# Performance work log

Hardware: AMD Instinct MI355X
Metric: run time of the kernel (lower is better)

## Reference

```python
import jax, jax.numpy as jnp
import numpy as np

N, E, D, R = 50000, 600000, 128, 8


def setup_inputs() -> dict:
    key = jax.random.key(0)
    ks = jax.random.split(key, 10)
    return {
        "x": jax.random.normal(ks[0], (N, D), dtype=jnp.float32),
        "h": jax.random.normal(ks[1], (N, D), dtype=jnp.float32),
        "edge_index": jax.random.randint(ks[2], (2, E), 0, N, dtype=jnp.int32),
        "edge_type": jax.random.randint(ks[3], (E,), 0, R, dtype=jnp.int32),
        "edge_weight": jax.random.uniform(ks[4], (E,), dtype=jnp.float32),
        "rel_weight": jax.random.normal(ks[5], (R, D, D), dtype=jnp.float32) * 0.05,
        "root_weight": jax.random.normal(ks[6], (D, D), dtype=jnp.float32) * 0.05,
        "bias": jax.random.normal(ks[7], (D,), dtype=jnp.float32) * 0.05,
        "skip_weight": jax.random.normal(ks[8], (D, D), dtype=jnp.float32) * 0.05,
        "skip_bias": jax.random.normal(ks[9], (D,), dtype=jnp.float32) * 0.05,
    }


def reference(x, h, edge_index, edge_type, edge_weight, rel_weight, root_weight, bias, skip_weight, skip_bias):
    # skip projection (nn.Linear: y = x W^T + b)
    skip = x @ skip_weight.T + skip_bias  # [N, D]

    src, dst = edge_index[0], edge_index[1]  # PyG: message from src (x_j), aggregated at dst

    # Transform every node by every relation once (R is small), then gather per edge.
    # Avoids per-edge [E, D, D] weight gather.
    h_rel = jnp.einsum('nd,rdf->nrf', h, rel_weight)  # [N, R, D]
    msg = h_rel[src, edge_type] * edge_weight[:, None]  # [E, D]

    agg = jax.ops.segment_sum(msg, dst, num_segments=h.shape[0])  # [N, D]

    out = agg + h @ root_weight + bias + skip
    return out
```

## Files before the change

kernel.cpp:

```cpp
#include <hip/hip_runtime.h>


constexpr int DIM  = 128;
constexpr int BM   = 64;
constexpr int KC   = 32;
constexpr int BPAD = 4;
constexpr int KTOT = 1280;
constexpr int SCAN_CHUNK = 2048;

typedef __attribute__((ext_vector_type(8))) short     short8v;
typedef __attribute__((ext_vector_type(8))) unsigned short ushort8v;
typedef __attribute__((ext_vector_type(4))) float     float4v;

__device__ __forceinline__ unsigned short f2bf(float x) {
    union { float f; unsigned u; } c; c.f = x;
    unsigned u = c.u;
    u += 0x7fffu + ((u >> 16) & 1u);
    return (unsigned short)(u >> 16);
}

__global__ __launch_bounds__(256) void zero_i32_kernel(int* __restrict__ p, int n)
{
    int i = blockIdx.x * 256 + threadIdx.x;
    if (i < n) p[i] = 0;
}

__global__ __launch_bounds__(256) void hist_kernel(
    const int* __restrict__ ei, int* __restrict__ counts, int E)
{
    int e = blockIdx.x * 256 + threadIdx.x;
    if (e < E) atomicAdd(&counts[ei[(long long)E + e]], 1);
}

__global__ __launch_bounds__(256) void scan1_kernel(
    const int* __restrict__ counts, int* __restrict__ local,
    int* __restrict__ blockSums, int N)
{
    __shared__ int sh[256];
    const int b = blockIdx.x, t = threadIdx.x;
    const int base = b * SCAN_CHUNK + t * 8;

    int v[8];
    int s = 0;
    #pragma unroll
    for (int j = 0; j < 8; ++j) {
        int idx = base + j;
        v[j] = (idx < N) ? counts[idx] : 0;
        s += v[j];
    }
    sh[t] = s;
    __syncthreads();
    for (int off = 1; off < 256; off <<= 1) {
        int x = (t >= off) ? sh[t - off] : 0;
        __syncthreads();
        sh[t] += x;
        __syncthreads();
    }
    int ex = sh[t] - s;
    if (t == 255) blockSums[b] = sh[255];
    #pragma unroll
    for (int j = 0; j < 8; ++j) {
        int idx = base + j;
        if (idx < N) { local[idx] = ex; ex += v[j]; }
    }
}

__global__ __launch_bounds__(1024) void scan2_kernel(int* __restrict__ bs, int nb)
{
    __shared__ int sh[1024];
    const int t = threadIdx.x;
    int v = (t < nb) ? bs[t] : 0;
    sh[t] = v;
    __syncthreads();
    for (int off = 1; off < 1024; off <<= 1) {
        int x = (t >= off) ? sh[t - off] : 0;
        __syncthreads();
        sh[t] += x;
        __syncthreads();
    }
    if (t < nb) bs[t] = sh[t] - v;
}

__global__ __launch_bounds__(256) void scan3_kernel(
    int* __restrict__ offsets, const int* __restrict__ blockSums,
    int* __restrict__ cursor, int N, int E)
{
    const int b = blockIdx.x, t = threadIdx.x;
    const int add = blockSums[b];
    #pragma unroll
    for (int j = 0; j < 8; ++j) {
        int idx = b * SCAN_CHUNK + j * 256 + t;
        if (idx < N) {
            int v = offsets[idx] + add;
            offsets[idx] = v;
            cursor[idx]  = v;
        }
    }
    if (b == 0 && t == 0) offsets[N] = E;
}

__global__ __launch_bounds__(256) void scatter_kernel(
    const int* __restrict__ ei, const int* __restrict__ et,
    const float* __restrict__ ew, int* __restrict__ cursor,
    int* __restrict__ spack, float* __restrict__ sw, int E)
{
    int e = blockIdx.x * 256 + threadIdx.x;
    if (e < E) {
        int pos = atomicAdd(&cursor[ei[(long long)E + e]], 1);
        spack[pos] = (ei[e] << 3) | (et[e] & 7);
        sw[pos]    = ew[e];
    }
}

__global__ __launch_bounds__(256) void accum_kernel(
    const int* __restrict__ spack, const float* __restrict__ sw,
    const float* __restrict__ h, const int* __restrict__ offsets,
    unsigned short* __restrict__ S, int N)
{
    const int n    = blockIdx.x * 4 + (threadIdx.x >> 6);
    const int lane = threadIdx.x & 63;
    if (n >= N) return;

    const int start = offsets[n];
    const int end   = offsets[n + 1];

    float2 acc[8];
    #pragma unroll
    for (int rr = 0; rr < 8; ++rr) acc[rr] = make_float2(0.f, 0.f);

    int o = start;
    for (; o + 2 <= end; o += 2) {
        const int   p0 = spack[o],     p1 = spack[o + 1];
        const float w0 = sw[o],        w1 = sw[o + 1];
        const float2 h0 = *reinterpret_cast<const float2*>(
            h + (size_t)(p0 >> 3) * DIM + lane * 2);
        const float2 h1 = *reinterpret_cast<const float2*>(
            h + (size_t)(p1 >> 3) * DIM + lane * 2);
        const int r0 = p0 & 7, r1 = p1 & 7;
        #pragma unroll
        for (int rr = 0; rr < 8; ++rr) {
            const float m0 = (rr == r0) ? w0 : 0.f;
            const float m1 = (rr == r1) ? w1 : 0.f;
            acc[rr].x += m0 * h0.x + m1 * h1.x;
            acc[rr].y += m0 * h0.y + m1 * h1.y;
        }
    }
    if (o < end) {
        const int   p0 = spack[o];
        const float w0 = sw[o];
        const float2 h0 = *reinterpret_cast<const float2*>(
            h + (size_t)(p0 >> 3) * DIM + lane * 2);
        const int r0 = p0 & 7;
        #pragma unroll
        for (int rr = 0; rr < 8; ++rr) {
            const float m0 = (rr == r0) ? w0 : 0.f;
            acc[rr].x += m0 * h0.x;
            acc[rr].y += m0 * h0.y;
        }
    }

    #pragma unroll
    for (int rr = 0; rr < 8; ++rr) {
        unsigned pk = (unsigned)f2bf(acc[rr].x) | ((unsigned)f2bf(acc[rr].y) << 16);
        *reinterpret_cast<unsigned*>(
            &S[(size_t)n * 1024 + rr * DIM + lane * 2]) = pk;
    }
}

__global__ __launch_bounds__(256) void repack_B_kernel(
    const float* __restrict__ relF, const float* __restrict__ rootW,
    const float* __restrict__ skipW, unsigned short* __restrict__ Bt)
{
    int idx = blockIdx.x * 256 + threadIdx.x;
    if (idx >= DIM * KTOT) return;
    int f = idx / KTOT, k = idx % KTOT;
    float v;
    if (k < 1024)       v = relF[(size_t)k * DIM + f];
    else if (k < 1152)  v = rootW[(k - 1024) * DIM + f];
    else                v = skipW[f * DIM + (k - 1152)];
    Bt[(size_t)f * KTOT + k] = f2bf(v);
}

__global__ __launch_bounds__(256) void mfma_gemm_kernel(
    const unsigned short* __restrict__ S, const float* __restrict__ h,
    const float* __restrict__ x, const unsigned short* __restrict__ Bt,
    const float* __restrict__ bias, const float* __restrict__ skipB,
    float* __restrict__ out, int N)
{
    __shared__ unsigned short As[128 * 64];
    __shared__ unsigned short Bs[128 * 64];

    const int tid  = threadIdx.x;
    const int lane = tid & 63;
    const int wid  = tid >> 6;
    const int wr   = wid >> 1, wc = wid & 1;
    const int l15  = lane & 15, l4 = lane >> 4;
    const int n0   = blockIdx.x * 128;

    float4v acc[4][4];
    #pragma unroll
    for (int m = 0; m < 4; ++m)
        #pragma unroll
        for (int nn = 0; nn < 4; ++nn)
            acc[m][nn] = (float4v)0.f;

    for (int k0 = 0; k0 < KTOT; k0 += 64) {
        __syncthreads();
        if (k0 < 1024) {
            #pragma unroll
            for (int i = 0; i < 4; ++i) {
                int idx = tid + i * 256;
                int row = idx >> 3, c8 = idx & 7;
                int n = n0 + row;
                ushort8v v = (ushort8v)0;
                if (n < N)
                    v = *reinterpret_cast<const ushort8v*>(
                        &S[(size_t)n * 1024 + k0 + c8 * 8]);
                int bo = row * 128 + ((c8 * 16) ^ ((row & 7) << 4));
                *reinterpret_cast<ushort8v*>((char*)As + bo) = v;
            }
        } else {
            const float* __restrict__ A = (k0 < 1152) ? h : x;
            const int kb = (k0 < 1152) ? (k0 - 1024) : (k0 - 1152);
            #pragma unroll
            for (int i = 0; i < 8; ++i) {
                int idx = tid + i * 256;
                int row = idx >> 4, c4 = idx & 15;
                int n = n0 + row;
                float4 v = make_float4(0.f, 0.f, 0.f, 0.f);
                if (n < N)
                    v = *reinterpret_cast<const float4*>(
                        &A[(size_t)n * DIM + kb + c4 * 4]);
                unsigned short b4[4] = { f2bf(v.x), f2bf(v.y), f2bf(v.z), f2bf(v.w) };
                int bo = row * 128 + ((c4 * 8) ^ ((row & 7) << 4));
                *reinterpret_cast<ulonglong1*>((char*)As + bo) =
                    *reinterpret_cast<const ulonglong1*>(b4);
            }
        }
        #pragma unroll
        for (int i = 0; i < 4; ++i) {
            int idx = tid + i * 256;
            int col = idx >> 3, c8 = idx & 7;
            ushort8v v = *reinterpret_cast<const ushort8v*>(
                &Bt[(size_t)col * KTOT + k0 + c8 * 8]);
            int bo = col * 128 + ((c8 * 16) ^ ((col & 7) << 4));
            *reinterpret_cast<ushort8v*>((char*)Bs + bo) = v;
        }
        __syncthreads();

        #pragma unroll
        for (int s = 0; s < 2; ++s) {
            const int kk = s * 32 + l4 * 8;
            short8v a[4], b[4];
            #pragma unroll
            for (int m = 0; m < 4; ++m) {
                int row = wr * 64 + m * 16 + l15;
                int bo = row * 128 + ((kk * 2) ^ ((row & 7) << 4));
                a[m] = *reinterpret_cast<const short8v*>((const char*)As + bo);
            }
            #pragma unroll
            for (int nn = 0; nn < 4; ++nn) {
                int col = wc * 64 + nn * 16 + l15;
                int bo = col * 128 + ((kk * 2) ^ ((col & 7) << 4));
                b[nn] = *reinterpret_cast<const short8v*>((const char*)Bs + bo);
            }
            #pragma unroll
            for (int m = 0; m < 4; ++m)
                #pragma unroll
                for (int nn = 0; nn < 4; ++nn)
                    acc[m][nn] = __builtin_amdgcn_mfma_f32_16x16x32_bf16(
                        a[m], b[nn], acc[m][nn], 0, 0, 0);
        }
    }

    #pragma unroll
    for (int nn = 0; nn < 4; ++nn) {
        const int col = wc * 64 + nn * 16 + l15;
        const float bb = bias[col] + skipB[col];
        #pragma unroll
        for (int m = 0; m < 4; ++m) {
            #pragma unroll
            for (int j = 0; j < 4; ++j) {
                int row = wr * 64 + m * 16 + l4 * 4 + j;
                int n = n0 + row;
                if (n < N)
                    out[(size_t)n * DIM + col] = acc[m][nn][j] + bb;
            }
        }
    }
}

__global__ __launch_bounds__(256) void base_kernel(
    const float* __restrict__ x, const float* __restrict__ h,
    const float* __restrict__ skipW, const float* __restrict__ rootW,
    const float* __restrict__ bias, const float* __restrict__ skipB,
    float* __restrict__ out, int N)
{
    __shared__ float As2[BM][KC];
    __shared__ float Bs2[KC][DIM + BPAD];

    const int tid = threadIdx.x;
    const int n0  = blockIdx.x * BM;
    const int f0  = (tid & 31) * 4;
    const int r0  = (tid >> 5) * 8;

    float acc[8][4] = {};

    for (int phase = 0; phase < 2; ++phase) {
        const float* __restrict__ A = phase ? h : x;
        for (int d0 = 0; d0 < DIM; d0 += KC) {
            __syncthreads();
            for (int idx = tid; idx < BM * KC; idx += 256) {
                int r = idx / KC, dd = idx % KC;
                int n = n0 + r;
                As2[r][dd] = (n < N) ? A[(long long)n * DIM + d0 + dd] : 0.f;
            }
            if (phase == 0) {
                for (int idx = tid; idx < DIM * KC; idx += 256) {
                    int f = idx / KC, dd = idx % KC;
                    Bs2[dd][f] = skipW[f * DIM + d0 + dd];
                }
            } else {
                for (int idx = tid; idx < KC * DIM; idx += 256) {
                    int dd = idx / DIM, f = idx % DIM;
                    Bs2[dd][f] = rootW[(d0 + dd) * DIM + f];
                }
            }
            __syncthreads();
            #pragma unroll
            for (int dd = 0; dd < KC; ++dd) {
                float a[8];
                #pragma unroll
                for (int i = 0; i < 8; ++i) a[i] = As2[r0 + i][dd];
                const float4 b = *reinterpret_cast<const float4*>(&Bs2[dd][f0]);
                #pragma unroll
                for (int i = 0; i < 8; ++i) {
                    acc[i][0] += a[i] * b.x; acc[i][1] += a[i] * b.y;
                    acc[i][2] += a[i] * b.z; acc[i][3] += a[i] * b.w;
                }
            }
        }
    }

    float bb[4];
    #pragma unroll
    for (int j = 0; j < 4; ++j) bb[j] = bias[f0 + j] + skipB[f0 + j];
    #pragma unroll
    for (int i = 0; i < 8; ++i) {
        int n = n0 + r0 + i;
        if (n < N) {
            float4 v = make_float4(acc[i][0] + bb[0], acc[i][1] + bb[1],
                                   acc[i][2] + bb[2], acc[i][3] + bb[3]);
            *reinterpret_cast<float4*>(&out[(long long)n * DIM + f0]) = v;
        }
    }
}

__global__ __launch_bounds__(256) void hrel_kernel(
    const float* __restrict__ h, const float* __restrict__ rel,
    float* __restrict__ hrel, int N, int R)
{
    __shared__ float As2[BM][KC];
    __shared__ float Bs2[KC][DIM + BPAD];

    const int tid = threadIdx.x;
    const int n0  = blockIdx.x * BM;
    const int rr  = blockIdx.y;
    const float* __restrict__ B = rel + (size_t)rr * DIM * DIM;
    const int f0  = (tid & 31) * 4;
    const int r0  = (tid >> 5) * 8;

    float acc[8][4] = {};

    for (int d0 = 0; d0 < DIM; d0 += KC) {
        __syncthreads();
        for (int idx = tid; idx < BM * KC; idx += 256) {
            int r = idx / KC, dd = idx % KC;
            int n = n0 + r;
            As2[r][dd] = (n < N) ? h[(long long)n * DIM + d0 + dd] : 0.f;
        }
        for (int idx = tid; idx < KC * DIM; idx += 256) {
            int dd = idx / DIM, f = idx % DIM;
            Bs2[dd][f] = B[(d0 + dd) * DIM + f];
        }
        __syncthreads();
        #pragma unroll
        for (int dd = 0; dd < KC; ++dd) {
            float a[8];
            #pragma unroll
            for (int i = 0; i < 8; ++i) a[i] = As2[r0 + i][dd];
            const float4 b = *reinterpret_cast<const float4*>(&Bs2[dd][f0]);
            #pragma unroll
            for (int i = 0; i < 8; ++i) {
                acc[i][0] += a[i] * b.x; acc[i][1] += a[i] * b.y;
                acc[i][2] += a[i] * b.z; acc[i][3] += a[i] * b.w;
            }
        }
    }

    #pragma unroll
    for (int i = 0; i < 8; ++i) {
        int n = n0 + r0 + i;
        if (n < N) {
            float4 v = make_float4(acc[i][0], acc[i][1], acc[i][2], acc[i][3]);
            *reinterpret_cast<float4*>(&hrel[((long long)n * R + rr) * DIM + f0]) = v;
        }
    }
}

__global__ __launch_bounds__(256) void edge_kernel(
    const int* __restrict__ ei, const int* __restrict__ et,
    const float* __restrict__ ew, const float* __restrict__ hrel,
    float* __restrict__ out, int E, int R)
{
    const int tid  = threadIdx.x;
    const int lane = tid & 31;
    const long long e = (long long)blockIdx.x * 8 + (tid >> 5);
    if (e >= E) return;

    const int   src = ei[e];
    const int   dst = ei[(long long)E + e];
    const int   r   = et[e];
    const float w   = ew[e];

    const float4 v = reinterpret_cast<const float4*>(
        hrel + ((long long)src * R + r) * DIM)[lane];

    float* o = out + (long long)dst * DIM + lane * 4;
    atomicAdd(o + 0, v.x * w);
    atomicAdd(o + 1, v.y * w);
    atomicAdd(o + 2, v.z * w);
    atomicAdd(o + 3, v.w * w);
}

__global__ __launch_bounds__(256) void edge_direct_kernel(
    const int* __restrict__ ei, const int* __restrict__ et,
    const float* __restrict__ ew, const float* __restrict__ h,
    const float* __restrict__ rel, float* __restrict__ out, int E)
{
    const int wid  = threadIdx.x >> 6;
    const int lane = threadIdx.x & 63;
    const long long e = (long long)blockIdx.x * 4 + wid;
    if (e >= E) return;

    const int   src = ei[e];
    const int   dst = ei[(long long)E + e];
    const int   r   = et[e];
    const float w   = ew[e];

    const float* __restrict__ hrow = h + (long long)src * DIM;
    const float* __restrict__ W    = rel + (size_t)r * DIM * DIM;

    float acc0 = 0.f, acc1 = 0.f;
    #pragma unroll 8
    for (int d = 0; d < DIM; ++d) {
        float hv = hrow[d];
        acc0 += hv * W[d * DIM + lane];
        acc1 += hv * W[d * DIM + lane + 64];
    }
    atomicAdd(&out[(long long)dst * DIM + lane],      acc0 * w);
    atomicAdd(&out[(long long)dst * DIM + lane + 64], acc1 * w);
}

extern "C" void kernel_launch(void* const* d_in, const int* in_sizes, int n_in,
                              void* d_out, int out_size, void* d_ws, size_t ws_size,
                              hipStream_t stream)
{
    const float* x     = (const float*)d_in[0];
    const float* h     = (const float*)d_in[1];
    const int*   ei    = (const int*)  d_in[2];
    const int*   et    = (const int*)  d_in[3];
    const float* ew    = (const float*)d_in[4];
    const float* rel   = (const float*)d_in[5];
    const float* rootW = (const float*)d_in[6];
    const float* bias  = (const float*)d_in[7];
    const float* skipW = (const float*)d_in[8];
    const float* skipB = (const float*)d_in[9];
    float* out = (float*)d_out;

    const int N = in_sizes[0] / DIM;
    const int E = in_sizes[3];
    const int R = in_sizes[5] / (DIM * DIM);

    const int nbScan = (N + SCAN_CHUNK - 1) / SCAN_CHUNK;

    const size_t S_elems  = (size_t)N * 1024;
    const size_t Bt_elems = (size_t)DIM * KTOT;
    const size_t need_new = S_elems * 2 + Bt_elems * 2
                          + ((size_t)(N + 1) + N + 1024 + E) * sizeof(int)
                          + (size_t)E * sizeof(float);

    if (R == 8 && nbScan <= 1024 && ws_size >= need_new) {
        unsigned short* S  = (unsigned short*)d_ws;
        unsigned short* Bt = S + S_elems;
        int*   offsets   = (int*)(Bt + Bt_elems);
        int*   cursor    = offsets + (N + 1);
        int*   blockSums = cursor + N;
        int*   spack     = blockSums + 1024;
        float* sw        = (float*)(spack + E);

        zero_i32_kernel<<<dim3((N + 255) / 256), 256, 0, stream>>>(cursor, N);
        hist_kernel<<<dim3((E + 255) / 256), 256, 0, stream>>>(ei, cursor, E);
        scan1_kernel<<<dim3(nbScan), 256, 0, stream>>>(cursor, offsets, blockSums, N);
        scan2_kernel<<<dim3(1), 1024, 0, stream>>>(blockSums, nbScan);
        scan3_kernel<<<dim3(nbScan), 256, 0, stream>>>(offsets, blockSums, cursor, N, E);
        scatter_kernel<<<dim3((E + 255) / 256), 256, 0, stream>>>(
            ei, et, ew, cursor, spack, sw, E);
        repack_B_kernel<<<dim3((DIM * KTOT + 255) / 256), 256, 0, stream>>>(
            rel, rootW, skipW, Bt);
        accum_kernel<<<dim3((N + 3) / 4), 256, 0, stream>>>(
            spack, sw, h, offsets, S, N);
        mfma_gemm_kernel<<<dim3((N + 127) / 128), 256, 0, stream>>>(
            S, h, x, Bt, bias, skipB, out, N);
    } else {
        base_kernel<<<dim3((N + BM - 1) / BM), 256, 0, stream>>>(
            x, h, skipW, rootW, bias, skipB, out, N);
        if (ws_size >= (size_t)N * R * DIM * sizeof(float)) {
            float* hrel = (float*)d_ws;
            hrel_kernel<<<dim3((N + BM - 1) / BM, R), 256, 0, stream>>>(h, rel, hrel, N, R);
            edge_kernel<<<dim3((E + 7) / 8), 256, 0, stream>>>(ei, et, ew, hrel, out, E, R);
        } else {
            edge_direct_kernel<<<dim3((E + 3) / 4), 256, 0, stream>>>(ei, et, ew, h, rel, out, E);
        }
    }
}
```

Baseline: 200.3 us.

## Bucket edges by (dst, relation) to drop per-edge relation masking in accumulation

The CSR sort key changes from destination node to (destination, relation), so each node's edges arrive grouped by relation. The accumulation kernel can then keep a single float2 accumulator per relation segment, instead of running a masked FMA over all 8 relation slots for every edge. Source index and weight are packed into one int2 payload, so each edge needs one load instead of two. In exchange the histogram, scan and cursor arrays grow eightfold (400K entries), which means more zeroing and scan work and more offset reads.

```diff
diff --git a/kernel.cpp b/kernel.cpp
--- a/kernel.cpp
+++ b/kernel.cpp
@@ -26,15 +26,16 @@
 }
 
 __global__ __launch_bounds__(256) void hist_kernel(
-    const int* __restrict__ ei, int* __restrict__ counts, int E)
+    const int* __restrict__ ei, const int* __restrict__ et,
+    int* __restrict__ counts, int E)
 {
     int e = blockIdx.x * 256 + threadIdx.x;
-    if (e < E) atomicAdd(&counts[ei[(long long)E + e]], 1);
+    if (e < E) atomicAdd(&counts[ei[(long long)E + e] * 8 + (et[e] & 7)], 1);
 }
 
 __global__ __launch_bounds__(256) void scan1_kernel(
     const int* __restrict__ counts, int* __restrict__ local,
-    int* __restrict__ blockSums, int N)
+    int* __restrict__ blockSums, int M)
 {
     __shared__ int sh[256];
     const int b = blockIdx.x, t = threadIdx.x;
@@ -45,7 +46,7 @@
     #pragma unroll
     for (int j = 0; j < 8; ++j) {
         int idx = base + j;
-        v[j] = (idx < N) ? counts[idx] : 0;
+        v[j] = (idx < M) ? counts[idx] : 0;
         s += v[j];
     }
     sh[t] = s;
@@ -61,7 +62,7 @@
     #pragma unroll
     for (int j = 0; j < 8; ++j) {
         int idx = base + j;
-        if (idx < N) { local[idx] = ex; ex += v[j]; }
+        if (idx < M) { local[idx] = ex; ex += v[j]; }
     }
 }
 
@@ -83,87 +84,76 @@
 
 __global__ __launch_bounds__(256) void scan3_kernel(
     int* __restrict__ offsets, const int* __restrict__ blockSums,
-    int* __restrict__ cursor, int N, int E)
+    int* __restrict__ cursor, int M, int E)
 {
     const int b = blockIdx.x, t = threadIdx.x;
     const int add = blockSums[b];
     #pragma unroll
     for (int j = 0; j < 8; ++j) {
         int idx = b * SCAN_CHUNK + j * 256 + t;
-        if (idx < N) {
+        if (idx < M) {
             int v = offsets[idx] + add;
             offsets[idx] = v;
             cursor[idx]  = v;
         }
     }
-    if (b == 0 && t == 0) offsets[N] = E;
+    if (b == 0 && t == 0) offsets[M] = E;
 }
 
 __global__ __launch_bounds__(256) void scatter_kernel(
     const int* __restrict__ ei, const int* __restrict__ et,
     const float* __restrict__ ew, int* __restrict__ cursor,
-    int* __restrict__ spack, float* __restrict__ sw, int E)
+    int2* __restrict__ payload, int E)
 {
     int e = blockIdx.x * 256 + threadIdx.x;
     if (e < E) {
-        int pos = atomicAdd(&cursor[ei[(long long)E + e]], 1);
-        spack[pos] = (ei[e] << 3) | (et[e] & 7);
-        sw[pos]    = ew[e];
+        int key = ei[(long long)E + e] * 8 + (et[e] & 7);
+        int pos = atomicAdd(&cursor[key], 1);
+        payload[pos] = make_int2(ei[e], __float_as_int(ew[e]));
     }
 }
 
 __global__ __launch_bounds__(256) void accum_kernel(
-    const int* __restrict__ spack, const float* __restrict__ sw,
-    const float* __restrict__ h, const int* __restrict__ offsets,
-    unsigned short* __restrict__ S, int N)
+    const int2* __restrict__ payload, const float* __restrict__ h,
+    const int* __restrict__ offsets, unsigned short* __restrict__ S, int N)
 {
     const int n    = blockIdx.x * 4 + (threadIdx.x >> 6);
     const int lane = threadIdx.x & 63;
     if (n >= N) return;
 
-    const int start = offsets[n];
-    const int end   = offsets[n + 1];
-
-    float2 acc[8];
-    #pragma unroll
-    for (int rr = 0; rr < 8; ++rr) acc[rr] = make_float2(0.f, 0.f);
-
-    int o = start;
-    for (; o + 2 <= end; o += 2) {
-        const int   p0 = spack[o],     p1 = spack[o + 1];
-        const float w0 = sw[o],        w1 = sw[o + 1];
-        const float2 h0 = *reinterpret_cast<const float2*>(
-            h + (size_t)(p0 >> 3) * DIM + lane * 2);
-        const float2 h1 = *reinterpret_cast<const float2*>(
-            h + (size_t)(p1 >> 3) * DIM + lane * 2);
-        const int r0 = p0 & 7, r1 = p1 & 7;
-        #pragma unroll
-        for (int rr = 0; rr < 8; ++rr) {
-            const float m0 = (rr == r0) ? w0 : 0.f;
-            const float m1 = (rr == r1) ? w1 : 0.f;
-            acc[rr].x += m0 * h0.x + m1 * h1.x;
-            acc[rr].y += m0 * h0.y + m1 * h1.y;
-        }
-    }
-    if (o < end) {
-        const int   p0 = spack[o];
-        const float w0 = sw[o];
-        const float2 h0 = *reinterpret_cast<const float2*>(
-            h + (size_t)(p0 >> 3) * DIM + lane * 2);
-        const int r0 = p0 & 7;
-        #pragma unroll
-        for (int rr = 0; rr < 8; ++rr) {
-            const float m0 = (rr == r0) ? w0 : 0.f;
-            acc[rr].x += m0 * h0.x;
-            acc[rr].y += m0 * h0.y;
-        }
-    }
-
-    #pragma unroll
-    for (int rr = 0; rr < 8; ++rr) {
-        unsigned pk = (unsigned)f2bf(acc[rr].x) | ((unsigned)f2bf(acc[rr].y) << 16);
+    const int segBase = n * 8;
+    int s1 = offsets[segBase];
+
+    for (int r = 0; r < 8; ++r) {
+        const int s0 = s1;
+        s1 = offsets[segBase + r + 1];
+
+        float accx = 0.f, accy = 0.f;
+        int o = s0;
+        for (; o + 2 <= s1; o += 2) {
+            const int2 p0 = payload[o];
+            const int2 p1 = payload[o + 1];
+            const float2 h0 = *reinterpret_cast<const float2*>(
+                h + (size_t)p0.x * DIM + lane * 2);
+            const float2 h1 = *reinterpret_cast<const float2*>(
+                h + (size_t)p1.x * DIM + lane * 2);
+            const float w0 = __int_as_float(p0.y);
+            const float w1 = __int_as_float(p1.y);
+            accx += w0 * h0.x + w1 * h1.x;
+            accy += w0 * h0.y + w1 * h1.y;
+        }
+        if (o < s1) {
+            const int2 p0 = payload[o];
+            const float2 h0 = *reinterpret_cast<const float2*>(
+                h + (size_t)p0.x * DIM + lane * 2);
+            const float w0 = __int_as_float(p0.y);
+            accx += w0 * h0.x;
+            accy += w0 * h0.y;
+        }
+
+        unsigned pk = (unsigned)f2bf(accx) | ((unsigned)f2bf(accy) << 16);
         *reinterpret_cast<unsigned*>(
-            &S[(size_t)n * 1024 + rr * DIM + lane * 2]) = pk;
+            &S[(size_t)n * 1024 + r * DIM + lane * 2]) = pk;
     }
 }
 
@@ -482,34 +472,34 @@
     const int E = in_sizes[3];
     const int R = in_sizes[5] / (DIM * DIM);
 
-    const int nbScan = (N + SCAN_CHUNK - 1) / SCAN_CHUNK;
+    const int M = N * 8;
+    const int nbScan = (M + SCAN_CHUNK - 1) / SCAN_CHUNK;
 
     const size_t S_elems  = (size_t)N * 1024;
     const size_t Bt_elems = (size_t)DIM * KTOT;
     const size_t need_new = S_elems * 2 + Bt_elems * 2
-                          + ((size_t)(N + 1) + N + 1024 + E) * sizeof(int)
-                          + (size_t)E * sizeof(float);
+                          + ((size_t)(M + 1) + M + 1024) * sizeof(int)
+                          + (size_t)E * sizeof(int2);
 
     if (R == 8 && nbScan <= 1024 && ws_size >= need_new) {
         unsigned short* S  = (unsigned short*)d_ws;
         unsigned short* Bt = S + S_elems;
         int*   offsets   = (int*)(Bt + Bt_elems);
-        int*   cursor    = offsets + (N + 1);
-        int*   blockSums = cursor + N;
-        int*   spack     = blockSums + 1024;
-        float* sw        = (float*)(spack + E);
-
-        zero_i32_kernel<<<dim3((N + 255) / 256), 256, 0, stream>>>(cursor, N);
-        hist_kernel<<<dim3((E + 255) / 256), 256, 0, stream>>>(ei, cursor, E);
-        scan1_kernel<<<dim3(nbScan), 256, 0, stream>>>(cursor, offsets, blockSums, N);
+        int*   cursor    = offsets + (M + 1);
+        int*   blockSums = cursor + M;
+        int2*  payload   = (int2*)(blockSums + 1024);
+
+        zero_i32_kernel<<<dim3((M + 255) / 256), 256, 0, stream>>>(cursor, M);
+        hist_kernel<<<dim3((E + 255) / 256), 256, 0, stream>>>(ei, et, cursor, E);
+        scan1_kernel<<<dim3(nbScan), 256, 0, stream>>>(cursor, offsets, blockSums, M);
         scan2_kernel<<<dim3(1), 1024, 0, stream>>>(blockSums, nbScan);
-        scan3_kernel<<<dim3(nbScan), 256, 0, stream>>>(offsets, blockSums, cursor, N, E);
+        scan3_kernel<<<dim3(nbScan), 256, 0, stream>>>(offsets, blockSums, cursor, M, E);
         scatter_kernel<<<dim3((E + 255) / 256), 256, 0, stream>>>(
-            ei, et, ew, cursor, spack, sw, E);
+            ei, et, ew, cursor, payload, E);
         repack_B_kernel<<<dim3((DIM * KTOT + 255) / 256), 256, 0, stream>>>(
             rel, rootW, skipW, Bt);
         accum_kernel<<<dim3((N + 3) / 4), 256, 0, stream>>>(
-            spack, sw, h, offsets, S, N);
+            payload, h, offsets, S, N);
         mfma_gemm_kernel<<<dim3((N + 127) / 128), 256, 0, stream>>>(
             S, h, x, Bt, bias, skipB, out, N);
     } else {
```

After: 204.1 us. Within noise of the previous version (+1.9%).
